# Kernel tuning notes

Measured on AMD Instinct MI355X. Metric: run time of the kernel, lower is better.

The kernel has to match this reference:

```python
import jax, jax.numpy as jnp
import numpy as np
import math

B, S, D, H = 8, 256, 4096, 16
HD = D // H  # 256 == S, so the module's transposed mask application is exactly elementwise


def setup_inputs() -> dict:
    key = jax.random.key(0)
    ks = jax.random.split(key, 12)
    sc = 1.0 / math.sqrt(D)
    inp = {
        "q": jax.random.normal(ks[0], (B, S, D), dtype=jnp.float32),
        "k": jax.random.normal(ks[1], (B, S, D), dtype=jnp.float32),
        "v": jax.random.normal(ks[2], (B, S, D), dtype=jnp.float32),
        "mask": jax.random.randint(ks[3], (B, S), 0, 2),
        "Wq": jax.random.normal(ks[4], (D, D), dtype=jnp.float32) * sc,
        "bq": jnp.zeros((D,), dtype=jnp.float32),
        "Wk": jax.random.normal(ks[5], (D, D), dtype=jnp.float32) * sc,
        "bk": jnp.zeros((D,), dtype=jnp.float32),
        "Wv": jax.random.normal(ks[6], (D, D), dtype=jnp.float32) * sc,
        "bv": jnp.zeros((D,), dtype=jnp.float32),
        "Wo": jax.random.normal(ks[7], (D, D), dtype=jnp.float32) * sc,
        "bo": jnp.zeros((D,), dtype=jnp.float32),
    }
    return inp


def reference(q, k, v, mask, Wq, bq, Wk, bk, Wv, bv, Wo, bo):
    def proj(x, W, b):
        # nn.Linear: x @ W.T + b ; then [B,S,H,HD] -> [B,H,S,HD]
        return (x @ W.T + b).reshape(B, S, H, HD).transpose(0, 2, 1, 3)

    qh = proj(q, Wq, bq)
    kh = proj(k, Wk, bk)
    vh = proj(v, Wv, bv)

    # torch: attn_mask = (mask==0).view(bs,1,1,-1).repeat(1,H,HD,1) -> [B,H,HD,S]
    # then where(attn_mask, 0, q) against q of shape [B,H,S,HD] (elementwise since HD==S)
    am = jnp.broadcast_to((mask == 0)[:, None, None, :], (B, H, HD, S))
    qh = jnp.where(am, 0.0, qh)
    kh = jnp.where(am, 0.0, kh)

    scale = 1.0 / math.sqrt(HD)
    scores = jnp.einsum('bhqd,bhkd->bhqk', qh, kh) * scale
    w = jax.nn.softmax(scores, axis=-1)
    out = jnp.einsum('bhqk,bhkd->bhqd', w, vh)
    out = out.transpose(0, 2, 1, 3).reshape(B, S, D)
    out = out * (D ** -0.5)
    return out @ Wo.T + bo
```

## Files before the change

### kernel.cpp

```cpp
#include <hip/hip_runtime.h>


typedef _Float16 f16;
typedef f16 f16x8 __attribute__((ext_vector_type(8)));
typedef float f32x4 __attribute__((ext_vector_type(4)));

__device__ __forceinline__ void g2lds(const f16* g, f16* l) {
  __builtin_amdgcn_global_load_lds((const __attribute__((address_space(1))) void*)g,
                                   (__attribute__((address_space(3))) void*)l, 16, 0, 0);
}

__device__ __forceinline__ void cvt8(const float* src, f16* dst, int i) {
  float4 a = *(const float4*)(src + i);
  float4 b = *(const float4*)(src + i + 4);
  f16x8 o;
  o[0] = (f16)a.x; o[1] = (f16)a.y; o[2] = (f16)a.z; o[3] = (f16)a.w;
  o[4] = (f16)b.x; o[5] = (f16)b.y; o[6] = (f16)b.z; o[7] = (f16)b.w;
  *(f16x8*)(dst + i) = o;
}

__global__ __launch_bounds__(256) void cvt_x(const float* __restrict__ q,
                                             const float* __restrict__ k,
                                             const float* __restrict__ v,
                                             f16* __restrict__ oq, f16* __restrict__ ok,
                                             f16* __restrict__ ov) {
  const float* src; f16* dst;
  if (blockIdx.y == 0)      { src = q; dst = oq; }
  else if (blockIdx.y == 1) { src = k; dst = ok; }
  else                      { src = v; dst = ov; }
  cvt8(src, dst, (blockIdx.x * 256 + threadIdx.x) * 8);
}

__global__ __launch_bounds__(256) void cvt_w(const float* __restrict__ a,
                                             const float* __restrict__ b,
                                             const float* __restrict__ c,
                                             const float* __restrict__ d,
                                             f16* __restrict__ oa, f16* __restrict__ ob,
                                             f16* __restrict__ oc, f16* __restrict__ od) {
  const float* src; f16* dst;
  if (blockIdx.y == 0)      { src = a; dst = oa; }
  else if (blockIdx.y == 1) { src = b; dst = ob; }
  else if (blockIdx.y == 2) { src = c; dst = oc; }
  else                      { src = d; dst = od; }
  cvt8(src, dst, (blockIdx.x * 256 + threadIdx.x) * 8);
}

__global__ __launch_bounds__(512, 2) void gemm256(
    const f16* __restrict__ Aq, const f16* __restrict__ Ak,
    const f16* __restrict__ Bq, const f16* __restrict__ Bk,
    const float* __restrict__ bq, const float* __restrict__ bk,
    const int* __restrict__ mask,
    f16* __restrict__ Qbh, f16* __restrict__ Kbh)
{
  __shared__ __align__(16) f16 lds[2][4][8192];
  const int tid = threadIdx.x;
  const int lane = tid & 63, wid = tid >> 6;
  const int wm = wid >> 2, wn = wid & 3;
  const int ln = lane & 15, lh = lane >> 4;
  const int lnx = ln & 7;
  const int K = 4096, NT = 64;

  const int seg = blockIdx.x >> 7;
  int inner = blockIdx.x & 127;
  inner = (inner & 7) * 16 + (inner >> 3);

  const f16* A   = (seg == 0) ? Aq : Ak;
  const f16* B   = (seg == 0) ? Bq : Bk;
  const float* bias = (seg == 0) ? bq : bk;
  const int bm = inner % 8, bn = inner / 8;

  const size_t Abase = (size_t)bm * 256 * K;
  const size_t Bbase = (size_t)bn * 256 * K;

  const int sr = tid >> 3;
  const int ss = (tid & 7) ^ (sr & 7);

#define STAGEC(tt, bb_, c)                                                       \
  do {                                                                           \
    const f16* base_ = ((c) < 2) ? A + Abase + (size_t)((c) * 128) * K           \
                                 : B + Bbase + (size_t)(((c) - 2) * 128) * K;    \
    f16* dst_ = &lds[bb_][c][0];                                                 \
    g2lds(base_ + (size_t)sr * K + ((tt) << 6) + ss * 8, dst_ + tid * 8);        \
    g2lds(base_ + (size_t)(64 + sr) * K + ((tt) << 6) + ss * 8,                  \
          dst_ + (512 + tid) * 8);                                               \
  } while (0)

  f32x4 acc[8][4] = {};
  f16x8 a03[4][2], a47[4][2], b01[2][2], b23[2][2];

  STAGEC(0, 0, 0); STAGEC(0, 0, 1); STAGEC(0, 0, 2); STAGEC(0, 0, 3);
  STAGEC(1, 1, 0);
  asm volatile("s_waitcnt vmcnt(2)" ::: "memory");
  __builtin_amdgcn_s_barrier();

  for (int t = 0; t < NT; ++t) {
    const int bb = t & 1;
    const f16* cA = &lds[bb][wm][0];
    const f16* cB = &lds[bb][2 + (wn >> 1)][0];
    const int brow = (wn & 1) * 64;

#pragma unroll
    for (int m = 0; m < 4; ++m)
#pragma unroll
      for (int ks = 0; ks < 2; ++ks)
        a03[m][ks] = *(const f16x8*)&cA[(m * 16 + ln) * 64 + ((ks * 4 + lh) ^ lnx) * 8];
#pragma unroll
    for (int n = 0; n < 2; ++n)
#pragma unroll
      for (int ks = 0; ks < 2; ++ks)
        b01[n][ks] = *(const f16x8*)&cB[(brow + n * 16 + ln) * 64 + ((ks * 4 + lh) ^ lnx) * 8];
    if (t + 1 < NT) {
      STAGEC(t + 1, bb ^ 1, 1); STAGEC(t + 1, bb ^ 1, 2); STAGEC(t + 1, bb ^ 1, 3);
    }
    __builtin_amdgcn_s_barrier();
    __builtin_amdgcn_s_setprio(1);
#pragma unroll
    for (int m = 0; m < 4; ++m)
#pragma unroll
      for (int n = 0; n < 2; ++n)
#pragma unroll
        for (int ks = 0; ks < 2; ++ks)
          acc[m][n] = __builtin_amdgcn_mfma_f32_16x16x32_f16(a03[m][ks], b01[n][ks], acc[m][n], 0, 0, 0);
    __builtin_amdgcn_s_setprio(0);
    __builtin_amdgcn_s_barrier();

#pragma unroll
    for (int n = 0; n < 2; ++n)
#pragma unroll
      for (int ks = 0; ks < 2; ++ks)
        b23[n][ks] = *(const f16x8*)&cB[(brow + 32 + n * 16 + ln) * 64 + ((ks * 4 + lh) ^ lnx) * 8];
    __builtin_amdgcn_s_barrier();
    __builtin_amdgcn_s_setprio(1);
#pragma unroll
    for (int m = 0; m < 4; ++m)
#pragma unroll
      for (int n = 0; n < 2; ++n)
#pragma unroll
        for (int ks = 0; ks < 2; ++ks)
          acc[m][2 + n] = __builtin_amdgcn_mfma_f32_16x16x32_f16(a03[m][ks], b23[n][ks], acc[m][2 + n], 0, 0, 0);
    __builtin_amdgcn_s_setprio(0);
    __builtin_amdgcn_s_barrier();

#pragma unroll
    for (int m = 0; m < 4; ++m)
#pragma unroll
      for (int ks = 0; ks < 2; ++ks)
        a47[m][ks] = *(const f16x8*)&cA[((64 + m * 16) + ln) * 64 + ((ks * 4 + lh) ^ lnx) * 8];
    __builtin_amdgcn_s_barrier();
    __builtin_amdgcn_s_setprio(1);
#pragma unroll
    for (int m = 0; m < 4; ++m)
#pragma unroll
      for (int n = 0; n < 2; ++n)
#pragma unroll
        for (int ks = 0; ks < 2; ++ks)
          acc[4 + m][n] = __builtin_amdgcn_mfma_f32_16x16x32_f16(a47[m][ks], b01[n][ks], acc[4 + m][n], 0, 0, 0);
    __builtin_amdgcn_s_setprio(0);
    __builtin_amdgcn_s_barrier();

    if (t + 2 < NT) {
      STAGEC(t + 2, bb, 0);
      asm volatile("s_waitcnt vmcnt(2)" ::: "memory");
    } else {
      asm volatile("s_waitcnt vmcnt(0)" ::: "memory");
    }
    __builtin_amdgcn_s_barrier();
    __builtin_amdgcn_s_setprio(1);
#pragma unroll
    for (int m = 0; m < 4; ++m)
#pragma unroll
      for (int n = 0; n < 2; ++n)
#pragma unroll
        for (int ks = 0; ks < 2; ++ks)
          acc[4 + m][2 + n] = __builtin_amdgcn_mfma_f32_16x16x32_f16(a47[m][ks], b23[n][ks], acc[4 + m][2 + n], 0, 0, 0);
    __builtin_amdgcn_s_setprio(0);
    __builtin_amdgcn_s_barrier();
  }
#undef STAGEC

#pragma unroll
  for (int mf = 0; mf < 8; ++mf)
#pragma unroll
    for (int nf = 0; nf < 4; ++nf)
#pragma unroll
      for (int i = 0; i < 4; ++i) {
        int R = bm * 256 + wm * 128 + mf * 16 + lh * 4 + i;
        int C = bn * 256 + wn * 64 + nf * 16 + ln;
        float v = acc[mf][nf][i];
        v += bias[C];
        v = mask[(R >> 8) * 256 + (C & 255)] ? v : 0.0f;
        f16* o = (seg == 0) ? Qbh : Kbh;
        o[(size_t)((R >> 8) * 16 + (C >> 8)) * 65536 +
          (size_t)(R & 255) * 256 + (C & 255)] = (f16)v;
      }
}

template<int EPI>
__global__ __launch_bounds__(512, 2) void gemm_dp(
    const f16* __restrict__ A, const f16* __restrict__ B,
    const float* __restrict__ bias, void* __restrict__ out,
    int M, int N, int K)
{
  __shared__ __align__(16) f16 lds[3 * 24576];
  const int tid = threadIdx.x;
  const int lane = tid & 63, wid = tid >> 6;
  const int wm = wid >> 2, wn = wid & 3;
  const int ln = lane & 15, lh = lane >> 4;
  const int bm = blockIdx.y, bn = blockIdx.x;

  const size_t Abase = (size_t)bm * 128 * K;
  const size_t Bbase = (size_t)bn * 256 * K;
  const int sr = tid >> 3;
  const int ss = (tid & 7) ^ (sr & 7);
  const int NT = K >> 6;

  f16* p0 = &lds[0];
  f16* p1 = &lds[24576];
  f16* p2 = &lds[2 * 24576];

#define STAGE(t_, bo_, part)                                                    \
  do {                                                                          \
    const int kt_ = (t_) << 6;                                                  \
    if ((part) == 0) {                                                          \
      g2lds(A + Abase + (size_t)sr * K + kt_ + ss * 8,         (bo_) + tid * 8);  \
      g2lds(B + Bbase + (size_t)sr * K + kt_ + ss * 8,         (bo_) + 8192 + tid * 8); \
      g2lds(B + Bbase + (size_t)(64 + sr) * K + kt_ + ss * 8,  (bo_) + 8192 + (512 + tid) * 8); \
    } else {                                                                    \
      g2lds(A + Abase + (size_t)(64 + sr) * K + kt_ + ss * 8,  (bo_) + (512 + tid) * 8); \
      g2lds(B + Bbase + (size_t)(128 + sr) * K + kt_ + ss * 8, (bo_) + 8192 + (1024 + tid) * 8); \
      g2lds(B + Bbase + (size_t)(192 + sr) * K + kt_ + ss * 8, (bo_) + 8192 + (1536 + tid) * 8); \
    }                                                                           \
  } while (0)

  const int lx = ln & 7;
  const int arow = (wm * 64 + ln) * 64;
  const int brow = (wn * 64 + ln) * 64;

#define LOADFRAGS(fa, fb, buf, ks)                                              \
  do {                                                                          \
    const f16* bA_ = (buf);                                                     \
    const f16* bB_ = (buf) + 8192;                                              \
    const int so_ = (((ks) * 4 + lh) ^ lx) * 8;                                 \
    _Pragma("unroll")                                                           \
    for (int mf = 0; mf < 4; ++mf)                                              \
      fa[mf] = *(const f16x8*)&bA_[arow + mf * 1024 + so_];                     \
    _Pragma("unroll")                                                           \
    for (int nf = 0; nf < 4; ++nf)                                              \
      fb[nf] = *(const f16x8*)&bB_[brow + nf * 1024 + so_];                     \
  } while (0)

#define MFMA16(fa, fb)                                                          \
  do {                                                                          \
    __builtin_amdgcn_s_setprio(1);                                              \
    _Pragma("unroll")                                                           \
    for (int mf = 0; mf < 4; ++mf)                                              \
      _Pragma("unroll")                                                         \
      for (int nf = 0; nf < 4; ++nf)                                            \
        acc[mf][nf] = __builtin_amdgcn_mfma_f32_16x16x32_f16(fa[mf], fb[nf],    \
                                                             acc[mf][nf], 0, 0, 0); \
    __builtin_amdgcn_s_setprio(0);                                              \
  } while (0)

  f32x4 acc[4][4] = {};
  f16x8 ca[4], cb[4], na[4], nb[4];

  STAGE(0, p0, 0); STAGE(0, p0, 1);
  STAGE(1, p1, 0); STAGE(1, p1, 1);
  asm volatile("s_waitcnt vmcnt(6)" ::: "memory");
  __builtin_amdgcn_s_barrier();
  asm volatile("" ::: "memory");
  LOADFRAGS(ca, cb, p0, 0);

  for (int t = 0; t < NT; ++t) {
    LOADFRAGS(na, nb, p0, 1);
    if (t + 2 < NT) { STAGE(t + 2, p2, 0); STAGE(t + 2, p2, 1); }
    MFMA16(ca, cb);

    if (t + 1 < NT) {
      if (t + 2 < NT) {
        asm volatile("s_waitcnt vmcnt(6)" ::: "memory");
      } else {
        asm volatile("s_waitcnt vmcnt(0)" ::: "memory");
      }
      __builtin_amdgcn_s_barrier();
      asm volatile("" ::: "memory");
      LOADFRAGS(ca, cb, p1, 0);
      MFMA16(na, nb);
      asm volatile("" ::: "memory");
      __builtin_amdgcn_s_barrier();
      asm volatile("" ::: "memory");
      f16* tp = p0; p0 = p1; p1 = p2; p2 = tp;
    } else {
      MFMA16(na, nb);
    }
  }
#undef STAGE
#undef LOADFRAGS
#undef MFMA16

#pragma unroll
  for (int mf = 0; mf < 4; ++mf)
#pragma unroll
    for (int nf = 0; nf < 4; ++nf)
#pragma unroll
      for (int i = 0; i < 4; ++i) {
        int R = bm * 128 + wm * 64 + mf * 16 + lh * 4 + i;
        int C = bn * 256 + wn * 64 + nf * 16 + ln;
        float v = acc[mf][nf][i];
        if (EPI == 1) {
          v += bias[R];
          ((f16*)out)[(size_t)(C >> 8) * 1048576 + (size_t)R * 256 + (C & 255)] = (f16)v;
        } else {
          v += bias[C];
          ((float*)out)[(size_t)R * N + C] = v;
        }
      }
}

__global__ __launch_bounds__(256) void attn_kernel(
    const f16* __restrict__ Q, const f16* __restrict__ Kt,
    const f16* __restrict__ Vt, f16* __restrict__ aout)
{
  __shared__ __align__(16) f16 tile[64 * 256];
  __shared__ __align__(16) f16 pbuf[64 * 256];
  const int tid = threadIdx.x;
  const int lane = tid & 63, w = tid >> 6;
  const int ln = lane & 15, lh = lane >> 4;
  const int bh = blockIdx.x >> 2, rb = blockIdx.x & 3;
  const int b = bh >> 4, h = bh & 15;
  const size_t hb = (size_t)bh * 65536;

  const int strow = tid >> 5;
  const int stsl  = (tid & 31) ^ (strow & 7);

  f16x8 aq[8];
  {
    const f16* qp = Q + hb + (size_t)(rb * 64 + w * 16 + ln) * 256;
#pragma unroll
    for (int ks = 0; ks < 8; ++ks)
      aq[ks] = *(const f16x8*)(qp + ks * 32 + lh * 8);
  }

  f32x4 sacc[16] = {};

  for (int kt = 0; kt < 4; ++kt) {
#pragma unroll
    for (int c = 0; c < 8; ++c) {
      int L = c * 256 + tid;
      int row = c * 8 + strow;
      g2lds(Kt + hb + (size_t)(kt * 64 + row) * 256 + stsl * 8, &tile[L * 8]);
    }
    __syncthreads();
#pragma unroll
    for (int nf = 0; nf < 4; ++nf) {
      f16x8 bf[8];
#pragma unroll
      for (int ks = 0; ks < 8; ++ks) {
        int r = nf * 16 + ln;
        int sl = (ks * 4 + lh) ^ (r & 7);
        bf[ks] = *(const f16x8*)&tile[r * 256 + sl * 8];
      }
#pragma unroll
      for (int ks = 0; ks < 8; ++ks)
        sacc[kt * 4 + nf] = __builtin_amdgcn_mfma_f32_16x16x32_f16(
            aq[ks], bf[ks], sacc[kt * 4 + nf], 0, 0, 0);
    }
    __syncthreads();
  }

  const float SC = 1.0f / 16.0f;
  float mrow[4] = {-1e30f, -1e30f, -1e30f, -1e30f};
#pragma unroll
  for (int t = 0; t < 16; ++t)
#pragma unroll
    for (int i = 0; i < 4; ++i) mrow[i] = fmaxf(mrow[i], sacc[t][i]);
#pragma unroll
  for (int i = 0; i < 4; ++i) {
    mrow[i] = fmaxf(mrow[i], __shfl_xor(mrow[i], 1));
    mrow[i] = fmaxf(mrow[i], __shfl_xor(mrow[i], 2));
    mrow[i] = fmaxf(mrow[i], __shfl_xor(mrow[i], 4));
    mrow[i] = fmaxf(mrow[i], __shfl_xor(mrow[i], 8));
  }
  float ssum[4] = {0.f, 0.f, 0.f, 0.f};
#pragma unroll
  for (int t = 0; t < 16; ++t)
#pragma unroll
    for (int i = 0; i < 4; ++i) {
      float p = __expf((sacc[t][i] - mrow[i]) * SC);
      sacc[t][i] = p;
      ssum[i] += p;
    }
#pragma unroll
  for (int i = 0; i < 4; ++i) {
    ssum[i] += __shfl_xor(ssum[i], 1);
    ssum[i] += __shfl_xor(ssum[i], 2);
    ssum[i] += __shfl_xor(ssum[i], 4);
    ssum[i] += __shfl_xor(ssum[i], 8);
  }
  float rs[4];
#pragma unroll
  for (int i = 0; i < 4; ++i) rs[i] = 1.0f / ssum[i];

#pragma unroll
  for (int t = 0; t < 16; ++t)
#pragma unroll
    for (int i = 0; i < 4; ++i) {
      int row = w * 16 + lh * 4 + i;
      int col = (t >> 2) * 64 + (t & 3) * 16 + ln;
      pbuf[row * 256 + (col ^ ((row & 7) << 3))] = (f16)(sacc[t][i] * rs[i]);
    }

  f16x8 pa[8];
  {
    int r = w * 16 + ln;
#pragma unroll
    for (int ks = 0; ks < 8; ++ks) {
      int col = ks * 32 + lh * 8;
      pa[ks] = *(const f16x8*)&pbuf[r * 256 + (col ^ ((r & 7) << 3))];
    }
  }

  for (int dt = 0; dt < 4; ++dt) {
#pragma unroll
    for (int c = 0; c < 8; ++c) {
      int L = c * 256 + tid;
      int row = c * 8 + strow;
      g2lds(Vt + hb + (size_t)(dt * 64 + row) * 256 + stsl * 8, &tile[L * 8]);
    }
    __syncthreads();
    f32x4 oacc[4] = {};
#pragma unroll
    for (int nf = 0; nf < 4; ++nf) {
      f16x8 bf[8];
#pragma unroll
      for (int ks = 0; ks < 8; ++ks) {
        int r = nf * 16 + ln;
        int sl = (ks * 4 + lh) ^ (r & 7);
        bf[ks] = *(const f16x8*)&tile[r * 256 + sl * 8];
      }
#pragma unroll
      for (int ks = 0; ks < 8; ++ks)
        oacc[nf] = __builtin_amdgcn_mfma_f32_16x16x32_f16(pa[ks], bf[ks], oacc[nf], 0, 0, 0);
    }
#pragma unroll
    for (int nf = 0; nf < 4; ++nf)
#pragma unroll
      for (int i = 0; i < 4; ++i) {
        int s = rb * 64 + w * 16 + lh * 4 + i;
        int d = dt * 64 + nf * 16 + ln;
        aout[(size_t)(b * 256 + s) * 4096 + h * 256 + d] = (f16)(oacc[nf][i] * 0.015625f);
      }
    __syncthreads();
  }
}

extern "C" void kernel_launch(void* const* d_in, const int* in_sizes, int n_in,
                              void* d_out, int out_size, void* d_ws, size_t ws_size,
                              hipStream_t stream) {
  const float* q  = (const float*)d_in[0];
  const float* k  = (const float*)d_in[1];
  const float* v  = (const float*)d_in[2];
  const int*   mk = (const int*)d_in[3];
  const float* Wq = (const float*)d_in[4];
  const float* bq = (const float*)d_in[5];
  const float* Wk = (const float*)d_in[6];
  const float* bk = (const float*)d_in[7];
  const float* Wv = (const float*)d_in[8];
  const float* bv = (const float*)d_in[9];
  const float* Wo = (const float*)d_in[10];
  const float* bo = (const float*)d_in[11];
  float* out = (float*)d_out;

  const size_t NQ = 2048ull * 4096;
  const size_t NW = 4096ull * 4096;
  f16* ws = (f16*)d_ws;
  f16* q16  = ws;
  f16* k16  = q16 + NQ;
  f16* v16  = k16 + NQ;
  f16* Wq16 = v16 + NQ;
  f16* Wk16 = Wq16 + NW;
  f16* Wv16 = Wk16 + NW;
  f16* Wo16 = Wv16 + NW;
  f16* Qbh  = Wo16 + NW;
  f16* Kbh  = Qbh + NQ;
  f16* Vt   = Kbh + NQ;
  f16* at16 = Vt + NQ;

  cvt_x<<<dim3(4096, 3), 256, 0, stream>>>(q, k, v, q16, k16, v16);
  cvt_w<<<dim3(8192, 4), 256, 0, stream>>>(Wq, Wk, Wv, Wo, Wq16, Wk16, Wv16, Wo16);

  gemm256<<<256, 512, 0, stream>>>(q16, k16, Wq16, Wk16, bq, bk, mk, Qbh, Kbh);
  gemm_dp<1><<<dim3(8, 32), 512, 0, stream>>>(Wv16, v16, bv, Vt, 4096, 2048, 4096);
  attn_kernel<<<512, 256, 0, stream>>>(Qbh, Kbh, Vt, at16);
  gemm_dp<2><<<dim3(16, 16), 512, 0, stream>>>(at16, Wo16, bo, out, 2048, 4096, 4096);
}
```

Before: 376.6 us.

## Software-pipeline LDS fragment reads across MFMA phases in both GEMM kernels

In the 256-tile QK projection GEMM, each LDS fragment read now overlaps the previous MFMA quadrant. The next tile's A03/B01 fragments are prefetched before the last quadrant's MFMAs, and the full-drain barriers between phases go away. The 128x256 GEMM used for the V and output projections is rebuilt the same way. It drops from triple-buffered LDS with split k-halves to double buffering with four MFMA quadrants and staggered global-to-LDS staging. The aim is to hide LDS latency behind MFMA work, at the cost of less staging depth in the 128 kernel and more live fragment registers.

```diff
diff --git a/kernel.cpp b/kernel.cpp
--- a/kernel.cpp
+++ b/kernel.cpp
@@ -44,6 +44,20 @@
   else                      { src = d; dst = od; }
   cvt8(src, dst, (blockIdx.x * 256 + threadIdx.x) * 8);
 }
+
+#define MFMA8x(ACC, FA, FB, MO, NO)                                             \
+  do {                                                                          \
+    __builtin_amdgcn_s_setprio(1);                                              \
+    _Pragma("unroll")                                                           \
+    for (int m_ = 0; m_ < (MO); ++m_)                                           \
+      _Pragma("unroll")                                                         \
+      for (int n_ = 0; n_ < (NO); ++n_)                                         \
+        _Pragma("unroll")                                                       \
+        for (int ks_ = 0; ks_ < 2; ++ks_)                                       \
+          ACC = __builtin_amdgcn_mfma_f32_16x16x32_f16(FA[m_][ks_], FB[n_][ks_],\
+                                                       ACC, 0, 0, 0);           \
+    __builtin_amdgcn_s_setprio(0);                                              \
+  } while (0)
 
 __global__ __launch_bounds__(512, 2) void gemm256(
     const f16* __restrict__ Aq, const f16* __restrict__ Ak,
@@ -71,7 +85,6 @@
 
   const size_t Abase = (size_t)bm * 256 * K;
   const size_t Bbase = (size_t)bn * 256 * K;
-
   const int sr = tid >> 3;
   const int ss = (tid & 7) ^ (sr & 7);
 
@@ -85,78 +98,55 @@
           dst_ + (512 + tid) * 8);                                               \
   } while (0)
 
+#define RD_A03(buf) do { _Pragma("unroll")                                       \
+  for (int m_ = 0; m_ < 4; ++m_) _Pragma("unroll")                               \
+    for (int k_ = 0; k_ < 2; ++k_)                                               \
+      a03[m_][k_] = *(const f16x8*)&(buf)[(m_ * 16 + ln) * 64 + ((k_ * 4 + lh) ^ lnx) * 8]; } while (0)
+#define RD_A47(buf) do { _Pragma("unroll")                                       \
+  for (int m_ = 0; m_ < 4; ++m_) _Pragma("unroll")                               \
+    for (int k_ = 0; k_ < 2; ++k_)                                               \
+      a47[m_][k_] = *(const f16x8*)&(buf)[((64 + m_ * 16) + ln) * 64 + ((k_ * 4 + lh) ^ lnx) * 8]; } while (0)
+#define RD_B01(buf) do { _Pragma("unroll")                                       \
+  for (int n_ = 0; n_ < 2; ++n_) _Pragma("unroll")                               \
+    for (int k_ = 0; k_ < 2; ++k_)                                               \
+      b01[n_][k_] = *(const f16x8*)&(buf)[(brow + n_ * 16 + ln) * 64 + ((k_ * 4 + lh) ^ lnx) * 8]; } while (0)
+#define RD_B23(buf) do { _Pragma("unroll")                                       \
+  for (int n_ = 0; n_ < 2; ++n_) _Pragma("unroll")                               \
+    for (int k_ = 0; k_ < 2; ++k_)                                               \
+      b23[n_][k_] = *(const f16x8*)&(buf)[(brow + 32 + n_ * 16 + ln) * 64 + ((k_ * 4 + lh) ^ lnx) * 8]; } while (0)
+
   f32x4 acc[8][4] = {};
   f16x8 a03[4][2], a47[4][2], b01[2][2], b23[2][2];
+  const int brow = (wn & 1) * 64;
 
   STAGEC(0, 0, 0); STAGEC(0, 0, 1); STAGEC(0, 0, 2); STAGEC(0, 0, 3);
   STAGEC(1, 1, 0);
   asm volatile("s_waitcnt vmcnt(2)" ::: "memory");
   __builtin_amdgcn_s_barrier();
+  {
+    const f16* cA0 = &lds[0][wm][0];
+    const f16* cB0 = &lds[0][2 + (wn >> 1)][0];
+    RD_A03(cA0); RD_B01(cB0);
+  }
 
   for (int t = 0; t < NT; ++t) {
     const int bb = t & 1;
     const f16* cA = &lds[bb][wm][0];
     const f16* cB = &lds[bb][2 + (wn >> 1)][0];
-    const int brow = (wn & 1) * 64;
-
-#pragma unroll
-    for (int m = 0; m < 4; ++m)
-#pragma unroll
-      for (int ks = 0; ks < 2; ++ks)
-        a03[m][ks] = *(const f16x8*)&cA[(m * 16 + ln) * 64 + ((ks * 4 + lh) ^ lnx) * 8];
-#pragma unroll
-    for (int n = 0; n < 2; ++n)
-#pragma unroll
-      for (int ks = 0; ks < 2; ++ks)
-        b01[n][ks] = *(const f16x8*)&cB[(brow + n * 16 + ln) * 64 + ((ks * 4 + lh) ^ lnx) * 8];
-    if (t + 1 < NT) {
-      STAGEC(t + 1, bb ^ 1, 1); STAGEC(t + 1, bb ^ 1, 2); STAGEC(t + 1, bb ^ 1, 3);
-    }
-    __builtin_amdgcn_s_barrier();
-    __builtin_amdgcn_s_setprio(1);
-#pragma unroll
-    for (int m = 0; m < 4; ++m)
-#pragma unroll
-      for (int n = 0; n < 2; ++n)
-#pragma unroll
-        for (int ks = 0; ks < 2; ++ks)
-          acc[m][n] = __builtin_amdgcn_mfma_f32_16x16x32_f16(a03[m][ks], b01[n][ks], acc[m][n], 0, 0, 0);
-    __builtin_amdgcn_s_setprio(0);
-    __builtin_amdgcn_s_barrier();
-
-#pragma unroll
-    for (int n = 0; n < 2; ++n)
-#pragma unroll
-      for (int ks = 0; ks < 2; ++ks)
-        b23[n][ks] = *(const f16x8*)&cB[(brow + 32 + n * 16 + ln) * 64 + ((ks * 4 + lh) ^ lnx) * 8];
-    __builtin_amdgcn_s_barrier();
-    __builtin_amdgcn_s_setprio(1);
-#pragma unroll
-    for (int m = 0; m < 4; ++m)
-#pragma unroll
-      for (int n = 0; n < 2; ++n)
-#pragma unroll
-        for (int ks = 0; ks < 2; ++ks)
-          acc[m][2 + n] = __builtin_amdgcn_mfma_f32_16x16x32_f16(a03[m][ks], b23[n][ks], acc[m][2 + n], 0, 0, 0);
-    __builtin_amdgcn_s_setprio(0);
-    __builtin_amdgcn_s_barrier();
-
-#pragma unroll
-    for (int m = 0; m < 4; ++m)
-#pragma unroll
-      for (int ks = 0; ks < 2; ++ks)
-        a47[m][ks] = *(const f16x8*)&cA[((64 + m * 16) + ln) * 64 + ((ks * 4 + lh) ^ lnx) * 8];
-    __builtin_amdgcn_s_barrier();
-    __builtin_amdgcn_s_setprio(1);
-#pragma unroll
-    for (int m = 0; m < 4; ++m)
-#pragma unroll
-      for (int n = 0; n < 2; ++n)
-#pragma unroll
-        for (int ks = 0; ks < 2; ++ks)
-          acc[4 + m][n] = __builtin_amdgcn_mfma_f32_16x16x32_f16(a47[m][ks], b01[n][ks], acc[4 + m][n], 0, 0, 0);
-    __builtin_amdgcn_s_setprio(0);
-    __builtin_amdgcn_s_barrier();
+    const f16* cAn = &lds[bb ^ 1][wm][0];
+    const f16* cBn = &lds[bb ^ 1][2 + (wn >> 1)][0];
+
+    if (t + 1 < NT) { STAGEC(t + 1, bb ^ 1, 1); STAGEC(t + 1, bb ^ 1, 2); STAGEC(t + 1, bb ^ 1, 3); }
+    RD_B23(cB);
+    __builtin_amdgcn_s_barrier();
+    MFMA8x(acc[m_][n_], a03, b01, 4, 2);
+
+    RD_A47(cA);
+    __builtin_amdgcn_s_barrier();
+    MFMA8x(acc[m_][2 + n_], a03, b23, 4, 2);
+
+    __builtin_amdgcn_s_barrier();
+    MFMA8x(acc[4 + m_][n_], a47, b01, 4, 2);
 
     if (t + 2 < NT) {
       STAGEC(t + 2, bb, 0);
@@ -164,19 +154,16 @@
     } else {
       asm volatile("s_waitcnt vmcnt(0)" ::: "memory");
     }
-    __builtin_amdgcn_s_barrier();
-    __builtin_amdgcn_s_setprio(1);
-#pragma unroll
-    for (int m = 0; m < 4; ++m)
-#pragma unroll
-      for (int n = 0; n < 2; ++n)
-#pragma unroll
-        for (int ks = 0; ks < 2; ++ks)
-          acc[4 + m][2 + n] = __builtin_amdgcn_mfma_f32_16x16x32_f16(a47[m][ks], b23[n][ks], acc[4 + m][2 + n], 0, 0, 0);
-    __builtin_amdgcn_s_setprio(0);
-    __builtin_amdgcn_s_barrier();
+    asm volatile("s_waitcnt lgkmcnt(0)" ::: "memory");
+    __builtin_amdgcn_s_barrier();
+    if (t + 1 < NT) { RD_A03(cAn); RD_B01(cBn); }
+    MFMA8x(acc[4 + m_][2 + n_], a47, b23, 4, 2);
   }
 #undef STAGEC
+#undef RD_A03
+#undef RD_A47
+#undef RD_B01
+#undef RD_B23
 
 #pragma unroll
   for (int mf = 0; mf < 8; ++mf)
@@ -196,16 +183,17 @@
 }
 
 template<int EPI>
-__global__ __launch_bounds__(512, 2) void gemm_dp(
+__global__ __launch_bounds__(512, 2) void gemm128(
     const f16* __restrict__ A, const f16* __restrict__ B,
     const float* __restrict__ bias, void* __restrict__ out,
     int M, int N, int K)
 {
-  __shared__ __align__(16) f16 lds[3 * 24576];
+  __shared__ __align__(16) f16 lds[2 * 24576];
   const int tid = threadIdx.x;
   const int lane = tid & 63, wid = tid >> 6;
   const int wm = wid >> 2, wn = wid & 3;
   const int ln = lane & 15, lh = lane >> 4;
+  const int lnx = ln & 7;
   const int bm = blockIdx.y, bn = blockIdx.x;
 
   const size_t Abase = (size_t)bm * 128 * K;
@@ -214,89 +202,73 @@
   const int ss = (tid & 7) ^ (sr & 7);
   const int NT = K >> 6;
 
-  f16* p0 = &lds[0];
-  f16* p1 = &lds[24576];
-  f16* p2 = &lds[2 * 24576];
-
-#define STAGE(t_, bo_, part)                                                    \
+  f16* buf0 = &lds[0];
+  f16* buf1 = &lds[24576];
+
+#define STG1(t_, bo_)                                                           \
   do {                                                                          \
     const int kt_ = (t_) << 6;                                                  \
-    if ((part) == 0) {                                                          \
-      g2lds(A + Abase + (size_t)sr * K + kt_ + ss * 8,         (bo_) + tid * 8);  \
-      g2lds(B + Bbase + (size_t)sr * K + kt_ + ss * 8,         (bo_) + 8192 + tid * 8); \
-      g2lds(B + Bbase + (size_t)(64 + sr) * K + kt_ + ss * 8,  (bo_) + 8192 + (512 + tid) * 8); \
-    } else {                                                                    \
-      g2lds(A + Abase + (size_t)(64 + sr) * K + kt_ + ss * 8,  (bo_) + (512 + tid) * 8); \
-      g2lds(B + Bbase + (size_t)(128 + sr) * K + kt_ + ss * 8, (bo_) + 8192 + (1024 + tid) * 8); \
-      g2lds(B + Bbase + (size_t)(192 + sr) * K + kt_ + ss * 8, (bo_) + 8192 + (1536 + tid) * 8); \
-    }                                                                           \
+    g2lds(A + Abase + (size_t)sr * K + kt_ + ss * 8,         (bo_) + tid * 8);  \
+    g2lds(A + Abase + (size_t)(64 + sr) * K + kt_ + ss * 8,  (bo_) + (512 + tid) * 8); \
   } while (0)
-
-  const int lx = ln & 7;
-  const int arow = (wm * 64 + ln) * 64;
-  const int brow = (wn * 64 + ln) * 64;
-
-#define LOADFRAGS(fa, fb, buf, ks)                                              \
+#define STG2(t_, bo_)                                                           \
   do {                                                                          \
-    const f16* bA_ = (buf);                                                     \
-    const f16* bB_ = (buf) + 8192;                                              \
-    const int so_ = (((ks) * 4 + lh) ^ lx) * 8;                                 \
-    _Pragma("unroll")                                                           \
-    for (int mf = 0; mf < 4; ++mf)                                              \
-      fa[mf] = *(const f16x8*)&bA_[arow + mf * 1024 + so_];                     \
-    _Pragma("unroll")                                                           \
-    for (int nf = 0; nf < 4; ++nf)                                              \
-      fb[nf] = *(const f16x8*)&bB_[brow + nf * 1024 + so_];                     \
+    const int kt_ = (t_) << 6;                                                  \
+    g2lds(B + Bbase + (size_t)sr * K + kt_ + ss * 8,         (bo_) + 8192 + tid * 8); \
+    g2lds(B + Bbase + (size_t)(64 + sr) * K + kt_ + ss * 8,  (bo_) + 8192 + (512 + tid) * 8); \
+    g2lds(B + Bbase + (size_t)(128 + sr) * K + kt_ + ss * 8, (bo_) + 8192 + (1024 + tid) * 8); \
+    g2lds(B + Bbase + (size_t)(192 + sr) * K + kt_ + ss * 8, (bo_) + 8192 + (1536 + tid) * 8); \
   } while (0)
 
-#define MFMA16(fa, fb)                                                          \
-  do {                                                                          \
-    __builtin_amdgcn_s_setprio(1);                                              \
-    _Pragma("unroll")                                                           \
-    for (int mf = 0; mf < 4; ++mf)                                              \
-      _Pragma("unroll")                                                         \
-      for (int nf = 0; nf < 4; ++nf)                                            \
-        acc[mf][nf] = __builtin_amdgcn_mfma_f32_16x16x32_f16(fa[mf], fb[nf],    \
-                                                             acc[mf][nf], 0, 0, 0); \
-    __builtin_amdgcn_s_setprio(0);                                              \
-  } while (0)
+#define RD_A(fa, buf, mo) do { _Pragma("unroll")                                 \
+  for (int m_ = 0; m_ < 2; ++m_) _Pragma("unroll")                               \
+    for (int k_ = 0; k_ < 2; ++k_)                                               \
+      fa[m_][k_] = *(const f16x8*)&(buf)[(wm * 64 + ((mo) + m_) * 16 + ln) * 64 + ((k_ * 4 + lh) ^ lnx) * 8]; } while (0)
+#define RD_B(fb, buf, no) do { _Pragma("unroll")                                 \
+  for (int n_ = 0; n_ < 2; ++n_) _Pragma("unroll")                               \
+    for (int k_ = 0; k_ < 2; ++k_)                                               \
+      fb[n_][k_] = *(const f16x8*)&(buf)[8192 + (wn * 64 + ((no) + n_) * 16 + ln) * 64 + ((k_ * 4 + lh) ^ lnx) * 8]; } while (0)
 
   f32x4 acc[4][4] = {};
-  f16x8 ca[4], cb[4], na[4], nb[4];
-
-  STAGE(0, p0, 0); STAGE(0, p0, 1);
-  STAGE(1, p1, 0); STAGE(1, p1, 1);
-  asm volatile("s_waitcnt vmcnt(6)" ::: "memory");
+  f16x8 a01[2][2], a23[2][2], b01[2][2], b23[2][2];
+
+  STG1(0, buf0); STG2(0, buf0);
+  STG1(1, buf1);
+  asm volatile("s_waitcnt vmcnt(2)" ::: "memory");
   __builtin_amdgcn_s_barrier();
-  asm volatile("" ::: "memory");
-  LOADFRAGS(ca, cb, p0, 0);
+  RD_A(a01, buf0, 0); RD_B(b01, buf0, 0);
 
   for (int t = 0; t < NT; ++t) {
-    LOADFRAGS(na, nb, p0, 1);
-    if (t + 2 < NT) { STAGE(t + 2, p2, 0); STAGE(t + 2, p2, 1); }
-    MFMA16(ca, cb);
-
-    if (t + 1 < NT) {
-      if (t + 2 < NT) {
-        asm volatile("s_waitcnt vmcnt(6)" ::: "memory");
-      } else {
-        asm volatile("s_waitcnt vmcnt(0)" ::: "memory");
-      }
-      __builtin_amdgcn_s_barrier();
-      asm volatile("" ::: "memory");
-      LOADFRAGS(ca, cb, p1, 0);
-      MFMA16(na, nb);
-      asm volatile("" ::: "memory");
-      __builtin_amdgcn_s_barrier();
-      asm volatile("" ::: "memory");
-      f16* tp = p0; p0 = p1; p1 = p2; p2 = tp;
+    f16* bb  = (t & 1) ? buf1 : buf0;
+    f16* bbn = (t & 1) ? buf0 : buf1;
+
+    if (t + 1 < NT) STG2(t + 1, bbn);
+    RD_B(b23, bb, 2);
+    __builtin_amdgcn_s_barrier();
+    MFMA8x(acc[m_][n_], a01, b01, 2, 2);
+
+    RD_A(a23, bb, 2);
+    __builtin_amdgcn_s_barrier();
+    MFMA8x(acc[m_][2 + n_], a01, b23, 2, 2);
+
+    __builtin_amdgcn_s_barrier();
+    MFMA8x(acc[2 + m_][n_], a23, b01, 2, 2);
+
+    if (t + 2 < NT) {
+      STG1(t + 2, bb);
+      asm volatile("s_waitcnt vmcnt(2)" ::: "memory");
     } else {
-      MFMA16(na, nb);
-    }
-  }
-#undef STAGE
-#undef LOADFRAGS
-#undef MFMA16
+      asm volatile("s_waitcnt vmcnt(0)" ::: "memory");
+    }
+    asm volatile("s_waitcnt lgkmcnt(0)" ::: "memory");
+    __builtin_amdgcn_s_barrier();
+    if (t + 1 < NT) { RD_A(a01, bbn, 0); RD_B(b01, bbn, 0); }
+    MFMA8x(acc[2 + m_][2 + n_], a23, b23, 2, 2);
+  }
+#undef STG1
+#undef STG2
+#undef RD_A
+#undef RD_B
 
 #pragma unroll
   for (int mf = 0; mf < 4; ++mf)
@@ -490,7 +462,7 @@
   cvt_w<<<dim3(8192, 4), 256, 0, stream>>>(Wq, Wk, Wv, Wo, Wq16, Wk16, Wv16, Wo16);
 
   gemm256<<<256, 512, 0, stream>>>(q16, k16, Wq16, Wk16, bq, bk, mk, Qbh, Kbh);
-  gemm_dp<1><<<dim3(8, 32), 512, 0, stream>>>(Wv16, v16, bv, Vt, 4096, 2048, 4096);
+  gemm128<1><<<dim3(8, 32), 512, 0, stream>>>(Wv16, v16, bv, Vt, 4096, 2048, 4096);
   attn_kernel<<<512, 256, 0, stream>>>(Qbh, Kbh, Vt, at16);
-  gemm_dp<2><<<dim3(16, 16), 512, 0, stream>>>(at16, Wo16, bo, out, 2048, 4096, 4096);
-}
+  gemm128<2><<<dim3(16, 16), 512, 0, stream>>>(at16, Wo16, bo, out, 2048, 4096, 4096);
+}
```

New measurement: 394.2 us. 4.7% more time.
